# Kernel optimization log

Measured on AMD Instinct MI355X. Metric: run time of the kernel, lower is better.

Reference implementation:

```python
import jax, jax.numpy as jnp
import numpy as np

SEQ_LEN = 8192
D_K = 128
NEG_BIG = 1000000000.0


def setup_inputs() -> dict:
    key = jax.random.key(0)
    kq, kk, kv = jax.random.split(key, 3)
    q = jax.random.normal(kq, (SEQ_LEN, D_K), dtype=jnp.float32)
    k = jax.random.normal(kk, (SEQ_LEN, D_K), dtype=jnp.float32)
    v = jax.random.normal(kv, (SEQ_LEN, D_K), dtype=jnp.float32)
    return {"q": q, "k": k, "v": v}


def reference(q, k, v):
    # q,k,v: (S, d). Naive attention with causal (look-ahead) mask, masked=True.
    d_k = q.shape[-1]
    scaled_logits = jnp.matmul(q, k.T) / jnp.sqrt(jnp.asarray(d_k, q.dtype))  # (S, S)
    look_ahead_mask = jnp.triu(jnp.ones((SEQ_LEN, SEQ_LEN), dtype=q.dtype), k=1)
    scaled_logits = scaled_logits - look_ahead_mask * NEG_BIG
    attn = jnp.matmul(jax.nn.softmax(scaled_logits, axis=-1), v)  # (S, d)
    return attn
```

## Files before the change

### kernel.cpp

```cpp
#include <hip/hip_runtime.h>
#include <hip/hip_bf16.h>
#include <math.h>

#define S_LEN 8192
#define DK    128
#define BM    128
#define BN    64
#define NQT   (S_LEN / BM)
#define SCALE2 (0.08838834764831845f * 1.4426950408889634f)
#define DEFER_THR 5.0f

typedef __bf16 bf16x8_t __attribute__((ext_vector_type(8)));
typedef __bf16 bf16x4_t __attribute__((ext_vector_type(4)));
typedef __bf16 bf16x2_t __attribute__((ext_vector_type(2)));
typedef float  floatx16 __attribute__((ext_vector_type(16)));
typedef unsigned uintx4 __attribute__((ext_vector_type(4)));
typedef _Float16 half_t;
typedef _Float16 halfx4 __attribute__((ext_vector_type(4)));
typedef _Float16 halfx2 __attribute__((ext_vector_type(2)));

#define GLD16(g, l) __builtin_amdgcn_global_load_lds(                      \
    (const __attribute__((address_space(1))) void*)(g),                    \
    (__attribute__((address_space(3))) void*)(l), 16, 0, 0)

__device__ __forceinline__ float fexp2(float x) {
#if __has_builtin(__builtin_amdgcn_exp2f)
  return __builtin_amdgcn_exp2f(x);
#else
  return exp2f(x);
#endif
}

__device__ __forceinline__ unsigned pack2(float a, float b) {
  bf16x2_t w; w[0] = (__bf16)a; w[1] = (__bf16)b;
  return __builtin_bit_cast(unsigned, w);
}

__device__ __forceinline__ void xswap(unsigned &x, unsigned &y) {
#if __has_builtin(__builtin_amdgcn_permlane32_swap)
  typedef unsigned v2u __attribute__((ext_vector_type(2)));
  v2u t = __builtin_amdgcn_permlane32_swap(x, y, false, false);
  x = t[0]; y = t[1];
#else
  const unsigned sx = (unsigned)__shfl_xor((int)x, 32);
  const unsigned sy = (unsigned)__shfl_xor((int)y, 32);
  const bool lo = ((threadIdx.x & 63) < 32);
  const unsigned nx = lo ? x : sy;
  const unsigned ny = lo ? sx : y;
  x = nx; y = ny;
#endif
}

__global__ __launch_bounds__(256) void prep_kv(const float* __restrict__ K,
                                               const float* __restrict__ V,
                                               __bf16* __restrict__ Kb,
                                               __bf16* __restrict__ Vt) {
  __shared__ __bf16 t[64][DK + 8];
  const int bx  = blockIdx.x;
  const int tid = threadIdx.x;
  if (bx < (S_LEN * DK) / (256 * 4)) {
    const int i = (bx * 256 + tid) * 4;
    float4 v = *(const float4*)&K[i];
    bf16x4_t b;
    b[0] = (__bf16)v.x; b[1] = (__bf16)v.y; b[2] = (__bf16)v.z; b[3] = (__bf16)v.w;
    *(bf16x4_t*)&Kb[i] = b;
    return;
  }
  const int key0 = (bx - (S_LEN * DK) / (256 * 4)) * 64;
  {
    const int r = tid >> 2, cg = (tid & 3) * 32;
    const float* vp = V + (size_t)(key0 + r) * DK + cg;
    #pragma unroll
    for (int i = 0; i < 8; ++i) {
      float4 v = ((const float4*)vp)[i];
      bf16x4_t b;
      b[0] = (__bf16)v.x; b[1] = (__bf16)v.y; b[2] = (__bf16)v.z; b[3] = (__bf16)v.w;
      *(bf16x4_t*)&t[r][cg + i * 4] = b;
    }
  }
  __syncthreads();
  const int d = tid >> 1, h = (tid & 1) * 32;
  __bf16* op = Vt + (size_t)d * S_LEN + key0 + h;
  #pragma unroll
  for (int jb = 0; jb < 4; ++jb) {
    bf16x8_t b;
    #pragma unroll
    for (int j = 0; j < 8; ++j) b[j] = t[h + jb * 8 + j][d];
    *(bf16x8_t*)&op[jb * 8] = b;
  }
}

__global__ __launch_bounds__(256, 2)
void fa_part(const float* __restrict__ Q, const __bf16* __restrict__ Kb,
             const __bf16* __restrict__ Vtg, float* __restrict__ Out,
             half_t* __restrict__ Opart, float* __restrict__ stats, int C) {
  __shared__ __align__(16) __bf16 Ks[2][BN * DK];
  __shared__ __align__(16) __bf16 Vts[2][DK * BN];

  const int tid  = threadIdx.x;
  const int wave = tid >> 6;
  const int lane = tid & 63;
  const int l31  = lane & 31;
  const int hh   = lane >> 5;

  const int qtile = (NQT - 1) - blockIdx.x;
  const int g     = blockIdx.y;
  const int nt    = 2 * qtile + 2;
  const int jb0   = g * C;
  if (jb0 >= nt) return;
  const int jb1 = (jb0 + C < nt) ? (jb0 + C) : nt;

  const int h2 = C >> 1;
  const int direct = (qtile < h2);
  const int ca = qtile / h2, cr = qtile - ca * h2;
  const int chunk = h2 * ca * (ca + 1) / 2 + cr * (ca + 1) - h2 + g;

  const int qw  = qtile * BM + wave * 32;
  const int myq = qw + l31;

  bf16x8_t qf[8];
  {
    const float* qrow = Q + (size_t)myq * DK + hh * 8;
    #pragma unroll
    for (int s = 0; s < 8; ++s) {
      float4 x = *(const float4*)(qrow + s * 16);
      float4 y = *(const float4*)(qrow + s * 16 + 4);
      bf16x8_t f;
      f[0]=(__bf16)(x.x*SCALE2); f[1]=(__bf16)(x.y*SCALE2);
      f[2]=(__bf16)(x.z*SCALE2); f[3]=(__bf16)(x.w*SCALE2);
      f[4]=(__bf16)(y.x*SCALE2); f[5]=(__bf16)(y.y*SCALE2);
      f[6]=(__bf16)(y.z*SCALE2); f[7]=(__bf16)(y.w*SCALE2);
      qf[s] = f;
    }
  }

  const __bf16* kp[4]; const __bf16* vp[4]; int loff[4];
  {
    const int ck = (lane & 15) ^ ((wave * 4 + (lane >> 4)) & 15);
    const int cv = (lane & 7) ^ ((lane >> 3) & 7);
    #pragma unroll
    for (int t = 0; t < 4; ++t) {
      const int rk = t * 16 + wave * 4 + (lane >> 4);
      kp[t] = Kb + ((size_t)(jb0 * BN + rk)) * DK + ck * 8;
      const int rv = t * 32 + wave * 8 + (lane >> 3);
      vp[t] = Vtg + (size_t)rv * S_LEN + jb0 * BN + cv * 8;
      loff[t] = t * 2048 + wave * 512;
    }
  }

  floatx16 o_acc[4];
  #pragma unroll
  for (int d = 0; d < 4; ++d)
    #pragma unroll
    for (int r = 0; r < 16; ++r) o_acc[d][r] = 0.f;
  float m_r = -INFINITY, l_r = 0.f;

  #pragma unroll
  for (int t = 0; t < 4; ++t) { GLD16(kp[t], &Ks[0][loff[t]]); kp[t] += BN * DK; }
  #pragma unroll
  for (int t = 0; t < 4; ++t) { GLD16(vp[t], &Vts[0][loff[t]]); vp[t] += BN; }
  __syncthreads();

  int cur = 0;
  for (int jb = jb0; jb < jb1; ++jb) {
    if (jb + 1 < jb1) {
      #pragma unroll
      for (int t = 0; t < 4; ++t) { GLD16(kp[t], &Ks[cur ^ 1][loff[t]]); kp[t] += BN * DK; }
      #pragma unroll
      for (int t = 0; t < 4; ++t) { GLD16(vp[t], &Vts[cur ^ 1][loff[t]]); vp[t] += BN; }
    }

    if (jb * 64 <= qw + 31) {
      const __bf16* Kc = Ks[cur];
      const __bf16* Vc = Vts[cur];

      floatx16 sv[2];
      __builtin_amdgcn_s_setprio(1);
      #pragma unroll
      for (int g1 = 0; g1 < 2; ++g1) {
        floatx16 acc;
        #pragma unroll
        for (int r = 0; r < 16; ++r) acc[r] = 0.f;
        const int row = g1 * 32 + l31;
        #pragma unroll
        for (int s = 0; s < 8; ++s) {
          bf16x8_t kf = *(const bf16x8_t*)
              &Kc[row * DK + (((s * 2 + hh) ^ (row & 15)) * 8)];
          acc = __builtin_amdgcn_mfma_f32_32x32x16_bf16(kf, qf[s], acc, 0, 0, 0);
        }
        sv[g1] = acc;
      }
      __builtin_amdgcn_s_setprio(0);

      if (jb * 64 + 63 > qw) {
        #pragma unroll
        for (int g1 = 0; g1 < 2; ++g1)
          #pragma unroll
          for (int r = 0; r < 16; ++r) {
            const int key = jb * 64 + g1 * 32 + (r & 3) + ((r >> 2) << 3) + (hh << 2);
            if (key > myq) sv[g1][r] = -1e30f;
          }
      }

      float pmx[4];
      #pragma unroll
      for (int i = 0; i < 4; ++i)
        pmx[i] = fmaxf(fmaxf(sv[0][i], sv[0][i + 4]),
                       fmaxf(sv[0][i + 8], sv[0][i + 12]));
      #pragma unroll
      for (int i = 0; i < 4; ++i)
        pmx[i] = fmaxf(pmx[i], fmaxf(fmaxf(sv[1][i], sv[1][i + 4]),
                                     fmaxf(sv[1][i + 8], sv[1][i + 12])));
      float pm = fmaxf(fmaxf(pmx[0], pmx[1]), fmaxf(pmx[2], pmx[3]));
      {
        unsigned b0 = __builtin_bit_cast(unsigned, pm), b1 = b0;
        xswap(b0, b1);
        pm = fmaxf(__builtin_bit_cast(float, b0), __builtin_bit_cast(float, b1));
      }

      if (__any(pm > m_r + DEFER_THR)) {
        const float mn = fmaxf(m_r, pm);
        const float al = fexp2(m_r - mn);
        m_r = mn; l_r *= al;
        #pragma unroll
        for (int d = 0; d < 4; ++d)
          #pragma unroll
          for (int r = 0; r < 16; ++r) o_acc[d][r] *= al;
      }

      float rsx[4] = {0.f, 0.f, 0.f, 0.f};
      #pragma unroll
      for (int g1 = 0; g1 < 2; ++g1)
        #pragma unroll
        for (int r = 0; r < 16; ++r) {
          const float pv = fexp2(sv[g1][r] - m_r);
          sv[g1][r] = pv;
          rsx[r & 3] += pv;
        }
      float rs = (rsx[0] + rsx[1]) + (rsx[2] + rsx[3]);
      {
        unsigned b0 = __builtin_bit_cast(unsigned, rs), b1 = b0;
        xswap(b0, b1);
        l_r += __builtin_bit_cast(float, b0) + __builtin_bit_cast(float, b1);
      }

      unsigned pk[4][4];
      #pragma unroll
      for (int g1 = 0; g1 < 2; ++g1) {
        unsigned W0 = pack2(sv[g1][0],  sv[g1][1]);
        unsigned W1 = pack2(sv[g1][2],  sv[g1][3]);
        unsigned W2 = pack2(sv[g1][4],  sv[g1][5]);
        unsigned W3 = pack2(sv[g1][6],  sv[g1][7]);
        unsigned W4 = pack2(sv[g1][8],  sv[g1][9]);
        unsigned W5 = pack2(sv[g1][10], sv[g1][11]);
        unsigned W6 = pack2(sv[g1][12], sv[g1][13]);
        unsigned W7 = pack2(sv[g1][14], sv[g1][15]);
        xswap(W0, W2); xswap(W1, W3);
        xswap(W4, W6); xswap(W5, W7);
        pk[g1*2+0][0]=W0; pk[g1*2+0][1]=W1; pk[g1*2+0][2]=W2; pk[g1*2+0][3]=W3;
        pk[g1*2+1][0]=W4; pk[g1*2+1][1]=W5; pk[g1*2+1][2]=W6; pk[g1*2+1][3]=W7;
      }

      __builtin_amdgcn_s_setprio(1);
      #pragma unroll
      for (int ks = 0; ks < 4; ++ks) {
        uintx4 u; u[0]=pk[ks][0]; u[1]=pk[ks][1]; u[2]=pk[ks][2]; u[3]=pk[ks][3];
        const bf16x8_t pf = __builtin_bit_cast(bf16x8_t, u);
        #pragma unroll
        for (int d = 0; d < 4; ++d) {
          const int row = d * 32 + l31;
          bf16x8_t vf = *(const bf16x8_t*)
              &Vc[row * BN + (((ks * 2 + hh) ^ (row & 7)) * 8)];
          o_acc[d] = __builtin_amdgcn_mfma_f32_32x32x16_bf16(vf, pf, o_acc[d], 0, 0, 0);
        }
      }
      __builtin_amdgcn_s_setprio(0);
    }

    __syncthreads();
    cur ^= 1;
  }

  if (direct) {
    const float inv = (l_r > 0.f) ? (1.0f / l_r) : 0.f;
    float* orow = Out + (size_t)myq * DK;
    #pragma unroll
    for (int d = 0; d < 4; ++d)
      #pragma unroll
      for (int mI = 0; mI < 4; ++mI) {
        float4 st;
        st.x = o_acc[d][mI*4+0] * inv; st.y = o_acc[d][mI*4+1] * inv;
        st.z = o_acc[d][mI*4+2] * inv; st.w = o_acc[d][mI*4+3] * inv;
        *(float4*)&orow[d * 32 + mI * 8 + hh * 4] = st;
      }
  } else {
    const float inv = (l_r > 0.f) ? (1.0f / l_r) : 0.f;
    half_t* orow = Opart + ((size_t)chunk * BM + wave * 32 + l31) * DK;
    #pragma unroll
    for (int d = 0; d < 4; ++d)
      #pragma unroll
      for (int mI = 0; mI < 4; ++mI) {
        halfx4 st;
        st[0] = (half_t)(o_acc[d][mI*4+0] * inv);
        st[1] = (half_t)(o_acc[d][mI*4+1] * inv);
        st[2] = (half_t)(o_acc[d][mI*4+2] * inv);
        st[3] = (half_t)(o_acc[d][mI*4+3] * inv);
        *(halfx4*)&orow[d * 32 + mI * 8 + hh * 4] = st;
      }
    if (hh == 0) {
      stats[((size_t)chunk * BM + wave * 32 + l31) * 2 + 0] = m_r;
      stats[((size_t)chunk * BM + wave * 32 + l31) * 2 + 1] = l_r;
    }
  }
}

__global__ __launch_bounds__(256)
void fa_reduce(const half_t* __restrict__ Opart, const float* __restrict__ stats,
               float* __restrict__ O, int C) {
  const int h2 = C >> 1;
  const int wave = threadIdx.x >> 6, lane = threadIdx.x & 63;
  const int row = h2 * BM + blockIdx.x * 4 + wave;
  const int qt = row >> 7, r = row & 127;

  const int a = qt / h2, rr = qt - a * h2;
  const int base = h2 * a * (a + 1) / 2 + rr * (a + 1) - h2;
  const int nch = (qt + h2) / h2;

  float M = -INFINITY;
  for (int g = 0; g < nch; ++g)
    M = fmaxf(M, stats[((size_t)(base + g) * BM + r) * 2]);

  float L = 0.f, ax = 0.f, ay = 0.f;
  for (int g = 0; g < nch; ++g) {
    const size_t sidx = (size_t)(base + g) * BM + r;
    const float m = stats[sidx * 2];
    const float wl = fexp2(m - M) * stats[sidx * 2 + 1];
    L += wl;
    halfx2 o = *(const halfx2*)&Opart[sidx * DK + lane * 2];
    ax += wl * (float)o[0]; ay += wl * (float)o[1];
  }
  const float inv = 1.f / L;
  float2 res; res.x = ax * inv; res.y = ay * inv;
  *(float2*)&O[(size_t)row * DK + lane * 2] = res;
}

extern "C" void kernel_launch(void* const* d_in, const int* in_sizes, int n_in,
                              void* d_out, int out_size, void* d_ws, size_t ws_size,
                              hipStream_t stream) {
  (void)in_sizes; (void)n_in; (void)out_size;
  const float* q = (const float*)d_in[0];
  const float* k = (const float*)d_in[1];
  const float* v = (const float*)d_in[2];
  float* out = (float*)d_out;

  const size_t conv_bytes = (size_t)S_LEN * DK * 2 * 2;
  const size_t per_chunk  = (size_t)BM * DK * 2 + 2 * BM * 4;

  int C = 2 * NQT; long long nc = 0;
  for (int c = 8; c < 2 * NQT; c += 2) {
    const int hh2 = c / 2;
    const int a = NQT / hh2, rr = NQT - a * hh2;
    const long long F64 = (long long)hh2 * a * (a + 1) / 2 + (long long)rr * (a + 1);
    const long long n = F64 - hh2;
    if (conv_bytes + (size_t)n * per_chunk <= ws_size) { C = c; nc = n; break; }
  }

  __bf16* Kb = (__bf16*)d_ws;
  __bf16* Vt = Kb + (size_t)S_LEN * DK;
  half_t* Opart = (half_t*)(Vt + (size_t)S_LEN * DK);
  float* stats = (float*)(Opart + (size_t)nc * BM * DK);

  prep_kv<<<(S_LEN * DK) / (256 * 4) + S_LEN / 64, 256, 0, stream>>>(k, v, Kb, Vt);

  const int gy = (2 * NQT + C - 1) / C;
  fa_part<<<dim3(NQT, gy), 256, 0, stream>>>(q, Kb, Vt, out, Opart, stats, C);

  if (nc > 0) {
    const int h2 = C / 2;
    const int nrows = (NQT - h2) * BM;
    fa_reduce<<<nrows / 4, 256, 0, stream>>>(Opart, stats, out, C);
  }
}
```

Baseline: 124.5 us.

## Single-buffer V tile with mid-iteration sync, batch LDS fragment loads, split V transpose

In the attention kernel, V is now single-buffered in LDS. Its load is issued at the start of each iteration and overlaps the QK^T and softmax work, with an added barrier before the PV matmul. This cuts LDS use, which may help occupancy. K and V fragments are preloaded into register arrays ahead of their MFMA chains so the LDS loads are batched. The V transpose prep kernel is split into four times as many smaller blocks. The extra barrier per iteration and the larger register arrays risk more stalls and register pressure.

```diff
diff --git a/kernel.cpp b/kernel.cpp
--- a/kernel.cpp
+++ b/kernel.cpp
@@ -51,14 +51,14 @@
 #endif
 }
 
+#define KBLOCKS ((S_LEN * DK) / (256 * 4))
 __global__ __launch_bounds__(256) void prep_kv(const float* __restrict__ K,
                                                const float* __restrict__ V,
                                                __bf16* __restrict__ Kb,
                                                __bf16* __restrict__ Vt) {
-  __shared__ __bf16 t[64][DK + 8];
   const int bx  = blockIdx.x;
   const int tid = threadIdx.x;
-  if (bx < (S_LEN * DK) / (256 * 4)) {
+  if (bx < KBLOCKS) {
     const int i = (bx * 256 + tid) * 4;
     float4 v = *(const float4*)&K[i];
     bf16x4_t b;
@@ -66,28 +66,27 @@
     *(bf16x4_t*)&Kb[i] = b;
     return;
   }
-  const int key0 = (bx - (S_LEN * DK) / (256 * 4)) * 64;
+  __shared__ __bf16 tl[64][34];
+  const int vblk = bx - KBLOCKS;
+  const int key0 = (vblk >> 2) * 64;
+  const int d0   = (vblk & 3) * 32;
   {
-    const int r = tid >> 2, cg = (tid & 3) * 32;
-    const float* vp = V + (size_t)(key0 + r) * DK + cg;
-    #pragma unroll
-    for (int i = 0; i < 8; ++i) {
-      float4 v = ((const float4*)vp)[i];
-      bf16x4_t b;
-      b[0] = (__bf16)v.x; b[1] = (__bf16)v.y; b[2] = (__bf16)v.z; b[3] = (__bf16)v.w;
-      *(bf16x4_t*)&t[r][cg + i * 4] = b;
+    const int r = tid >> 2, fb = tid & 3;
+    const float* vp = V + (size_t)(key0 + r) * DK + d0;
+    #pragma unroll
+    for (int h = 0; h < 2; ++h) {
+      const int f = fb + h * 4;
+      float4 v = *(const float4*)(vp + f * 4);
+      tl[r][f * 4 + 0] = (__bf16)v.x; tl[r][f * 4 + 1] = (__bf16)v.y;
+      tl[r][f * 4 + 2] = (__bf16)v.z; tl[r][f * 4 + 3] = (__bf16)v.w;
     }
   }
   __syncthreads();
-  const int d = tid >> 1, h = (tid & 1) * 32;
-  __bf16* op = Vt + (size_t)d * S_LEN + key0 + h;
+  const int d = tid >> 3, kg = tid & 7;
+  bf16x8_t b;
   #pragma unroll
-  for (int jb = 0; jb < 4; ++jb) {
-    bf16x8_t b;
-    #pragma unroll
-    for (int j = 0; j < 8; ++j) b[j] = t[h + jb * 8 + j][d];
-    *(bf16x8_t*)&op[jb * 8] = b;
-  }
+  for (int j = 0; j < 8; ++j) b[j] = tl[kg * 8 + j][d];
+  *(bf16x8_t*)&Vt[(size_t)(d0 + d) * S_LEN + key0 + kg * 8] = b;
 }
 
 __global__ __launch_bounds__(256, 2)
@@ -95,7 +94,7 @@
              const __bf16* __restrict__ Vtg, float* __restrict__ Out,
              half_t* __restrict__ Opart, float* __restrict__ stats, int C) {
   __shared__ __align__(16) __bf16 Ks[2][BN * DK];
-  __shared__ __align__(16) __bf16 Vts[2][DK * BN];
+  __shared__ __align__(16) __bf16 Vts[DK * BN];
 
   const int tid  = threadIdx.x;
   const int wave = tid >> 6;
@@ -157,37 +156,43 @@
 
   #pragma unroll
   for (int t = 0; t < 4; ++t) { GLD16(kp[t], &Ks[0][loff[t]]); kp[t] += BN * DK; }
-  #pragma unroll
-  for (int t = 0; t < 4; ++t) { GLD16(vp[t], &Vts[0][loff[t]]); vp[t] += BN; }
   __syncthreads();
 
   int cur = 0;
   for (int jb = jb0; jb < jb1; ++jb) {
+    #pragma unroll
+    for (int t = 0; t < 4; ++t) { GLD16(vp[t], &Vts[loff[t]]); vp[t] += BN; }
     if (jb + 1 < jb1) {
       #pragma unroll
       for (int t = 0; t < 4; ++t) { GLD16(kp[t], &Ks[cur ^ 1][loff[t]]); kp[t] += BN * DK; }
-      #pragma unroll
-      for (int t = 0; t < 4; ++t) { GLD16(vp[t], &Vts[cur ^ 1][loff[t]]); vp[t] += BN; }
-    }
-
-    if (jb * 64 <= qw + 31) {
+    }
+
+    const int active = (jb * 64 <= qw + 31);
+    floatx16 sv[2];
+    unsigned pk[4][4];
+
+    if (active) {
       const __bf16* Kc = Ks[cur];
-      const __bf16* Vc = Vts[cur];
-
-      floatx16 sv[2];
+
+      bf16x8_t tf[16];
+      #pragma unroll
+      for (int g1 = 0; g1 < 2; ++g1) {
+        const int row = g1 * 32 + l31;
+        #pragma unroll
+        for (int s = 0; s < 8; ++s)
+          tf[g1 * 8 + s] = *(const bf16x8_t*)
+              &Kc[row * DK + (((s * 2 + hh) ^ (row & 15)) * 8)];
+      }
       __builtin_amdgcn_s_setprio(1);
       #pragma unroll
       for (int g1 = 0; g1 < 2; ++g1) {
         floatx16 acc;
         #pragma unroll
         for (int r = 0; r < 16; ++r) acc[r] = 0.f;
-        const int row = g1 * 32 + l31;
-        #pragma unroll
-        for (int s = 0; s < 8; ++s) {
-          bf16x8_t kf = *(const bf16x8_t*)
-              &Kc[row * DK + (((s * 2 + hh) ^ (row & 15)) * 8)];
-          acc = __builtin_amdgcn_mfma_f32_32x32x16_bf16(kf, qf[s], acc, 0, 0, 0);
-        }
+        #pragma unroll
+        for (int s = 0; s < 8; ++s)
+          acc = __builtin_amdgcn_mfma_f32_32x32x16_bf16(tf[g1 * 8 + s], qf[s],
+                                                        acc, 0, 0, 0);
         sv[g1] = acc;
       }
       __builtin_amdgcn_s_setprio(0);
@@ -244,7 +249,6 @@
         l_r += __builtin_bit_cast(float, b0) + __builtin_bit_cast(float, b1);
       }
 
-      unsigned pk[4][4];
       #pragma unroll
       for (int g1 = 0; g1 < 2; ++g1) {
         unsigned W0 = pack2(sv[g1][0],  sv[g1][1]);
@@ -260,19 +264,29 @@
         pk[g1*2+0][0]=W0; pk[g1*2+0][1]=W1; pk[g1*2+0][2]=W2; pk[g1*2+0][3]=W3;
         pk[g1*2+1][0]=W4; pk[g1*2+1][1]=W5; pk[g1*2+1][2]=W6; pk[g1*2+1][3]=W7;
       }
-
+    }
+
+    __syncthreads();
+
+    if (active) {
+      bf16x8_t vf[16];
+      #pragma unroll
+      for (int ks = 0; ks < 4; ++ks)
+        #pragma unroll
+        for (int d = 0; d < 4; ++d) {
+          const int row = d * 32 + l31;
+          vf[ks * 4 + d] = *(const bf16x8_t*)
+              &Vts[row * BN + (((ks * 2 + hh) ^ (row & 7)) * 8)];
+        }
       __builtin_amdgcn_s_setprio(1);
       #pragma unroll
       for (int ks = 0; ks < 4; ++ks) {
         uintx4 u; u[0]=pk[ks][0]; u[1]=pk[ks][1]; u[2]=pk[ks][2]; u[3]=pk[ks][3];
         const bf16x8_t pf = __builtin_bit_cast(bf16x8_t, u);
         #pragma unroll
-        for (int d = 0; d < 4; ++d) {
-          const int row = d * 32 + l31;
-          bf16x8_t vf = *(const bf16x8_t*)
-              &Vc[row * BN + (((ks * 2 + hh) ^ (row & 7)) * 8)];
-          o_acc[d] = __builtin_amdgcn_mfma_f32_32x32x16_bf16(vf, pf, o_acc[d], 0, 0, 0);
-        }
+        for (int d = 0; d < 4; ++d)
+          o_acc[d] = __builtin_amdgcn_mfma_f32_32x32x16_bf16(vf[ks * 4 + d], pf,
+                                                             o_acc[d], 0, 0, 0);
       }
       __builtin_amdgcn_s_setprio(0);
     }
@@ -370,7 +384,7 @@
   half_t* Opart = (half_t*)(Vt + (size_t)S_LEN * DK);
   float* stats = (float*)(Opart + (size_t)nc * BM * DK);
 
-  prep_kv<<<(S_LEN * DK) / (256 * 4) + S_LEN / 64, 256, 0, stream>>>(k, v, Kb, Vt);
+  prep_kv<<<KBLOCKS + 512, 256, 0, stream>>>(k, v, Kb, Vt);
 
   const int gy = (2 * NQT + C - 1) / C;
   fa_part<<<dim3(NQT, gy), 256, 0, stream>>>(q, Kb, Vt, out, Opart, stats, C);
```

After: 124.9 us. About the same (+0.3%).
